# Kernel optimization log

Hardware: AMD Instinct MI355X
Metric: run time of the kernel (lower is better)

## Reference

```python
import jax, jax.numpy as jnp
import numpy as np
import math

E = 1024   # embedding_dim
H = 16     # num_attention_heads
DH = 64    # head_embedding_dim
THD = H * DH
EPS = 1e-5

def _layernorm(x, g, b):
    m = jnp.mean(x, axis=-1, keepdims=True)
    v = jnp.mean(jnp.square(x - m), axis=-1, keepdims=True)
    return (x - m) * jax.lax.rsqrt(v + EPS) * g + b

def setup_inputs() -> dict:
    key = jax.random.key(0)
    ks = jax.random.split(key, 16)
    s_in = 1.0 / math.sqrt(E)
    s_o = 1.0 / math.sqrt(THD)
    inp = {"tokens": jax.random.normal(ks[0], (2, 2048, E), dtype=jnp.float32)}
    # q_linear / k_linear / v_linear: LayerNorm(E) then Linear(E -> THD)
    for i, name in enumerate(["q", "k", "v"]):
        inp[f"ln_{name}_g"] = jnp.ones((E,), jnp.float32)
        inp[f"ln_{name}_b"] = jnp.zeros((E,), jnp.float32)
        inp[f"W{name}"] = jax.random.uniform(ks[1 + 2 * i], (E, THD), jnp.float32, -s_in, s_in)
        inp[f"b{name}"] = jax.random.uniform(ks[2 + 2 * i], (THD,), jnp.float32, -s_in, s_in)
    # attention_linear: LayerNorm(THD) then Linear(THD -> E)
    inp["ln_o_g"] = jnp.ones((THD,), jnp.float32)
    inp["ln_o_b"] = jnp.zeros((THD,), jnp.float32)
    inp["Wo"] = jax.random.uniform(ks[7], (THD, E), jnp.float32, -s_o, s_o)
    inp["bo"] = jax.random.uniform(ks[8], (E,), jnp.float32, -s_o, s_o)
    return inp

def reference(tokens, ln_q_g, ln_q_b, Wq, bq, ln_k_g, ln_k_b, Wk, bk,
              ln_v_g, ln_v_b, Wv, bv, ln_o_g, ln_o_b, Wo, bo):
    N, L, _ = tokens.shape
    # NOTE: faithful to source quirk -- k comes from v_linear, v comes from k_linear.
    q = (_layernorm(tokens, ln_q_g, ln_q_b) @ Wq + bq).reshape(N, L, H, DH).transpose(0, 2, 1, 3)  # (N,H,L,Dh)
    k = (_layernorm(tokens, ln_v_g, ln_v_b) @ Wv + bv).reshape(N, L, H, DH).transpose(0, 2, 3, 1)  # (N,H,Dh,L)
    v = (_layernorm(tokens, ln_k_g, ln_k_b) @ Wk + bk).reshape(N, L, H, DH).transpose(0, 2, 1, 3)  # (N,H,L,Dh)
    qkT = jnp.einsum('bhid,bhdj->bhij', q, k)  # (N,H,L,L)
    # mask added BEFORE dividing by sqrt(Dh), as in source
    mask = jnp.triu(jnp.full((L, L), -9999.0, dtype=qkT.dtype), k=1)
    attn = jax.nn.softmax((qkT + mask) / math.sqrt(DH), axis=-1)
    wv = jnp.einsum('bhij,bhjd->bhid', attn, v).transpose(0, 2, 1, 3).reshape(N, L, THD)
    out = _layernorm(wv, ln_o_g, ln_o_b) @ Wo + bo + tokens
    return (out, k, v)
```

## Files before the change

kernel.cpp:

```cpp
#include <hip/hip_runtime.h>

#define L_SEQ 2048
#define NH    16
#define E_DIM 1024
#define M_ROWS 4096

typedef unsigned short u16;
typedef unsigned int   u32;
typedef __attribute__((ext_vector_type(8))) __bf16 bf16x8;
typedef __attribute__((ext_vector_type(4))) float  f32x4;

__device__ __forceinline__ u16 f2bf(float f) {
  union { float f; u32 u; } x; x.f = f;
  u32 u = x.u;
  return (u16)((u + 0x7FFFu + ((u >> 16) & 1u)) >> 16);
}
__device__ __forceinline__ float bf2f(u16 v) {
  union { u32 u; float f; } x; x.u = ((u32)v) << 16;
  return x.f;
}
__device__ __forceinline__ void st_bf4(u16* p, float a, float b, float c, float d) {
  ushort4 u; u.x = f2bf(a); u.y = f2bf(b); u.z = f2bf(c); u.w = f2bf(d);
  *reinterpret_cast<ushort4*>(p) = u;
}
__device__ __forceinline__ u32 pktrunc(float a, float b) {
  union { float f; u32 u; } xa, xb; xa.f = a; xb.f = b;
  return (xa.u >> 16) | (xb.u & 0xFFFF0000u);
}
__device__ __forceinline__ void gload16(const u16* g, u16* l) {
  __builtin_amdgcn_global_load_lds(
      (const __attribute__((address_space(1))) void*)g,
      (__attribute__((address_space(3))) void*)l, 16, 0, 0);
}
#define SBAR() asm volatile("s_barrier" ::: "memory")

__global__ __launch_bounds__(256) void ln_hat_f32(const float* __restrict__ x, u16* __restrict__ o)
{
  __shared__ float red[8];
  const size_t row = blockIdx.x;
  const int t = threadIdx.x;
  float4 v = reinterpret_cast<const float4*>(x + row * E_DIM)[t];
  float s = v.x + v.y + v.z + v.w;
  float q = v.x*v.x + v.y*v.y + v.z*v.z + v.w*v.w;
  #pragma unroll
  for (int off = 32; off; off >>= 1) { s += __shfl_down(s, off); q += __shfl_down(q, off); }
  if ((t & 63) == 0) { red[t >> 6] = s; red[4 + (t >> 6)] = q; }
  __syncthreads();
  float S = red[0] + red[1] + red[2] + red[3];
  float Q = red[4] + red[5] + red[6] + red[7];
  float mean = S * (1.f / E_DIM);
  float rstd = rsqrtf(Q * (1.f / E_DIM) - mean * mean + 1e-5f);
  st_bf4(o + row * E_DIM + t * 4,
         (v.x - mean) * rstd, (v.y - mean) * rstd, (v.z - mean) * rstd, (v.w - mean) * rstd);
}

__global__ __launch_bounds__(256) void ln_hat_bf16(const u16* __restrict__ x, u16* __restrict__ o)
{
  __shared__ float red[8];
  const size_t row = blockIdx.x;
  const int t = threadIdx.x;
  ushort4 u = reinterpret_cast<const ushort4*>(x + row * E_DIM)[t];
  float v0 = bf2f(u.x), v1 = bf2f(u.y), v2 = bf2f(u.z), v3 = bf2f(u.w);
  float s = v0 + v1 + v2 + v3;
  float q = v0*v0 + v1*v1 + v2*v2 + v3*v3;
  #pragma unroll
  for (int off = 32; off; off >>= 1) { s += __shfl_down(s, off); q += __shfl_down(q, off); }
  if ((t & 63) == 0) { red[t >> 6] = s; red[4 + (t >> 6)] = q; }
  __syncthreads();
  float S = red[0] + red[1] + red[2] + red[3];
  float Q = red[4] + red[5] + red[6] + red[7];
  float mean = S * (1.f / E_DIM);
  float rstd = rsqrtf(Q * (1.f / E_DIM) - mean * mean + 1e-5f);
  st_bf4(o + row * E_DIM + t * 4,
         (v0 - mean) * rstd, (v1 - mean) * rstd, (v2 - mean) * rstd, (v3 - mean) * rstd);
}

__global__ __launch_bounds__(256) void transpose_all(
    const float* __restrict__ W0, const float* __restrict__ W1,
    const float* __restrict__ W2, const float* __restrict__ W3,
    const float* __restrict__ g0, const float* __restrict__ g1,
    const float* __restrict__ g2, const float* __restrict__ g3,
    u16* __restrict__ T0, u16* __restrict__ T1, u16* __restrict__ T2, u16* __restrict__ T3)
{
  __shared__ float tile[32][33];
  const int z = blockIdx.z;
  const float* W = (z == 0) ? W0 : (z == 1) ? W1 : (z == 2) ? W2 : W3;
  const float* g = (z == 0) ? g0 : (z == 1) ? g1 : (z == 2) ? g2 : g3;
  u16* T = (z == 0) ? T0 : (z == 1) ? T1 : (z == 2) ? T2 : T3;
  const int tx = threadIdx.x & 31, ty = threadIdx.x >> 5;
  const int bx = blockIdx.x * 32, by = blockIdx.y * 32;
  #pragma unroll
  for (int r = 0; r < 4; ++r) {
    const int e = by + ty + r * 8;
    tile[ty + r * 8][tx] = W[(size_t)e * E_DIM + bx + tx] * g[e];
  }
  __syncthreads();
  #pragma unroll
  for (int r = 0; r < 4; ++r)
    T[(size_t)(bx + ty + r * 8) * E_DIM + by + tx] = f2bf(tile[tx][ty + r * 8]);
}

__global__ __launch_bounds__(256) void bias_fold(
    const float* __restrict__ W0, const float* __restrict__ W1,
    const float* __restrict__ W2, const float* __restrict__ W3,
    const float* __restrict__ l0, const float* __restrict__ l1,
    const float* __restrict__ l2, const float* __restrict__ l3,
    const float* __restrict__ b0, const float* __restrict__ b1,
    const float* __restrict__ b2, const float* __restrict__ b3,
    float* __restrict__ bfold)
{
  __shared__ float part[8][32];
  const int z = blockIdx.y;
  const float* W  = (z == 0) ? W0 : (z == 1) ? W1 : (z == 2) ? W2 : W3;
  const float* bl = (z == 0) ? l0 : (z == 1) ? l1 : (z == 2) ? l2 : l3;
  const float* bs = (z == 0) ? b0 : (z == 1) ? b1 : (z == 2) ? b2 : b3;
  const int tn = threadIdx.x & 31, te = threadIdx.x >> 5;
  const int n = blockIdx.x * 32 + tn;
  float acc = 0.f;
  const int e0 = te * 128;
  for (int e = e0; e < e0 + 128; ++e) acc += bl[e] * W[(size_t)e * E_DIM + n];
  part[te][tn] = acc;
  __syncthreads();
  if (te == 0) {
    float s = part[0][tn] + part[1][tn] + part[2][tn] + part[3][tn]
            + part[4][tn] + part[5][tn] + part[6][tn] + part[7][tn];
    bfold[z * E_DIM + n] = bs[n] + s;
  }
}

#define GBK 64
__device__ __forceinline__ void core128(
    const u16* __restrict__ A, const u16* __restrict__ BT,
    int m0, int n0, int t, u16* lds, f32x4 (&acc)[4][4])
{
  const int lane = t & 63, wave = t >> 6;
  const int wm = wave >> 1, wn = wave & 1;
  const int fr = lane & 15, hi = lane >> 4;
  const int sx = fr & 7;

  auto STAGE = [&](int buf, int kt) {
    u16* la = lds + (buf * 2 + 0) * (128 * GBK);
    u16* lb = lds + (buf * 2 + 1) * (128 * GBK);
    #pragma unroll
    for (int s = 0; s < 4; ++s) {
      const int seg = t + s * 256;
      const int r = seg >> 3;
      const int gc = (seg & 7) ^ (r & 7);
      gload16(A + (size_t)(m0 + r) * E_DIM + kt * GBK + gc * 8, la + seg * 8);
    }
    #pragma unroll
    for (int s = 0; s < 4; ++s) {
      const int seg = t + s * 256;
      const int r = seg >> 3;
      const int gc = (seg & 7) ^ (r & 7);
      gload16(BT + (size_t)(n0 + r) * E_DIM + kt * GBK + gc * 8, lb + seg * 8);
    }
  };
  auto AF = [&](int buf, int i, int ks) -> bf16x8 {
    return *reinterpret_cast<const bf16x8*>(
        lds + (buf * 2 + 0) * (128 * GBK) + (wm * 64 + i * 16 + fr) * GBK + (((ks * 4 + hi) ^ sx) * 8));
  };
  auto BF = [&](int buf, int j, int ks) -> bf16x8 {
    return *reinterpret_cast<const bf16x8*>(
        lds + (buf * 2 + 1) * (128 * GBK) + (wn * 64 + j * 16 + fr) * GBK + (((ks * 4 + hi) ^ sx) * 8));
  };
  auto PHASES = [&](int buf) {
    bf16x8 a[4][2], b[4][2];
    #pragma unroll
    for (int i = 0; i < 4; ++i) { a[i][0] = AF(buf, i, 0); a[i][1] = AF(buf, i, 1); }
    #pragma unroll
    for (int j = 0; j < 4; ++j) { b[j][0] = BF(buf, j, 0); b[j][1] = BF(buf, j, 1); }
    __builtin_amdgcn_s_setprio(1);
    #pragma unroll
    for (int i = 0; i < 4; ++i)
      #pragma unroll
      for (int j = 0; j < 4; ++j) {
        acc[i][j] = __builtin_amdgcn_mfma_f32_16x16x32_bf16(a[i][0], b[j][0], acc[i][j], 0, 0, 0);
        acc[i][j] = __builtin_amdgcn_mfma_f32_16x16x32_bf16(a[i][1], b[j][1], acc[i][j], 0, 0, 0);
      }
    __builtin_amdgcn_s_setprio(0);
  };

  STAGE(0, 0);
  #pragma unroll 1
  for (int kt = 0; kt < 15; ++kt) {
    const int buf = kt & 1;
    SBAR();
    STAGE(buf ^ 1, kt + 1);
    asm volatile("s_waitcnt vmcnt(8)" ::: "memory");
    SBAR();
    PHASES(buf);
  }
  asm volatile("s_waitcnt vmcnt(0)" ::: "memory");
  SBAR();
  PHASES(1);
}

__global__ __launch_bounds__(256, 2) void gemm_qkv128(
    const u16* __restrict__ xhat, const u16* __restrict__ WTcat,
    const float* __restrict__ bfold,
    float* __restrict__ kout, float* __restrict__ vout,
    u16* __restrict__ qbf, u16* __restrict__ kbf, u16* __restrict__ vTb)
{
  __shared__ u16 lds[4 * 128 * GBK];
  const int t = threadIdx.x;
  const int xcd = blockIdx.x & 7, l = blockIdx.x >> 3;
  const int by = 8 * (xcd >> 1) + l / 12;
  const int bx = 12 * (xcd & 1) + l % 12;
  const int m0 = by * 128, n0 = bx * 128;

  f32x4 acc[4][4] = {};
  core128(xhat, WTcat, m0, n0, t, lds, acc);

  const int lane = t & 63, wave = t >> 6;
  const int wm = wave >> 1, wn = wave & 1;
  const int fr = lane & 15, hi = lane >> 4;
  const int z = n0 >> 10;
  const float* bias = bfold + z * E_DIM;
  const int rowb = hi * 4;
  #pragma unroll
  for (int i = 0; i < 4; ++i) {
    const int mbase = m0 + wm * 64 + i * 16 + rowb;
    #pragma unroll
    for (int j = 0; j < 4; ++j) {
      const int ng = n0 + wn * 64 + j * 16 + fr;
      const int ncol = ng & 1023;
      const float bval = bias[ncol];
      #pragma unroll
      for (int r = 0; r < 4; ++r) {
        const int m = mbase + r;
        const float val = acc[i][j][r] + bval;
        const int b = m >> 11, ltok = m & 2047, h = ncol >> 6, d = ncol & 63;
        const size_t bh = (size_t)(b * NH + h);
        if (z == 0) {
          qbf[((bh * L_SEQ + ltok) << 6) + d] = f2bf(val);
        } else if (z == 1) {
          kout[(bh * 64 + d) * L_SEQ + ltok] = val;
          kbf[((bh * L_SEQ + ltok) << 6) + d] = f2bf(val);
        } else {
          vout[(bh * L_SEQ + ltok) * 64 + d] = val;
          vTb[(bh * 64 + d) * L_SEQ + ltok] = f2bf(val);
        }
      }
    }
  }
}

__global__ __launch_bounds__(256, 2) void gemm_o128(
    const u16* __restrict__ A, const u16* __restrict__ BT, const float* __restrict__ bias,
    const float* __restrict__ tokens, float* __restrict__ out)
{
  __shared__ u16 lds[4 * 128 * GBK];
  const int t = threadIdx.x;
  const int xcd = blockIdx.x & 7, l = blockIdx.x >> 3;
  const int by = 8 * (xcd >> 1) + (l >> 2);
  const int bx = 4 * (xcd & 1) + (l & 3);
  const int m0 = by * 128, n0 = bx * 128;

  f32x4 acc[4][4] = {};
  core128(A, BT, m0, n0, t, lds, acc);

  const int lane = t & 63, wave = t >> 6;
  const int wm = wave >> 1, wn = wave & 1;
  const int fr = lane & 15, hi = lane >> 4;
  const int rowb = hi * 4;
  #pragma unroll
  for (int i = 0; i < 4; ++i) {
    const int mbase = m0 + wm * 64 + i * 16 + rowb;
    #pragma unroll
    for (int j = 0; j < 4; ++j) {
      const int ncol = n0 + wn * 64 + j * 16 + fr;
      const float bval = bias[ncol];
      #pragma unroll
      for (int r = 0; r < 4; ++r) {
        const int m = mbase + r;
        out[(size_t)m * E_DIM + ncol] = acc[i][j][r] + bval + tokens[(size_t)m * E_DIM + ncol];
      }
    }
  }
}

__global__ __launch_bounds__(256) void attn_mfma(
    const u16* __restrict__ qbf, const u16* __restrict__ kbf,
    const u16* __restrict__ vTb, u16* __restrict__ wv)
{
  __shared__ u16 Klds[64][72];
  __shared__ u16 Vlds[64][72];
  __shared__ u16 Plds[4][16][72];
  const int t = threadIdx.x, lane = t & 63, wave = t >> 6;
  const int bi = blockIdx.x;
  const int bh = (bi & 7) + 8 * ((bi >> 3) & 3);
  const int pr = bi >> 5;
  const int fr = lane & 15, hi = lane >> 4;
  const u16* kbase = kbf + (size_t)bh * L_SEQ * 64;
  const u16* vbase = vTb + (size_t)bh * 64 * L_SEQ;
  const int b = bh >> 4, h = bh & 15;
  const float kSC2  = 0.125f * 1.44269504089f;
  const float kMSK2 = -1803.2f;

  #pragma unroll 1
  for (int half = 0; half < 2; ++half) {
    const int qt = half ? (31 - pr) : pr;
    const int q0w = qt * 64 + wave * 16;
    const int qg = q0w + fr;

    const u16* qrow = qbf + ((size_t)bh * L_SEQ + q0w + fr) * 64 + hi * 8;
    const bf16x8 qf0 = *reinterpret_cast<const bf16x8*>(qrow);
    const bf16x8 qf1 = *reinterpret_cast<const bf16x8*>(qrow + 32);

    f32x4 o[4] = {};
    float mrun = -3.0e38f, lrun = 0.f;

    for (int tkv = 0; tkv <= qt; ++tkv) {
      const int j0 = tkv * 64;
      const bool diag = (tkv == qt);
      #pragma unroll
      for (int s = 0; s < 2; ++s) {
        const int seg = t + s * 256;
        const int r = seg >> 3, c8 = (seg & 7) * 8;
        *reinterpret_cast<uint4*>(&Klds[r][c8]) =
            *reinterpret_cast<const uint4*>(kbase + (size_t)(j0 + r) * 64 + c8);
        *reinterpret_cast<uint4*>(&Vlds[r][c8]) =
            *reinterpret_cast<const uint4*>(vbase + (size_t)r * L_SEQ + j0 + c8);
      }
      __syncthreads();

      f32x4 st[4] = {};
      __builtin_amdgcn_s_setprio(1);
      #pragma unroll
      for (int kt = 0; kt < 4; ++kt) {
        bf16x8 ka0 = *reinterpret_cast<const bf16x8*>(&Klds[kt*16 + fr][hi*8]);
        bf16x8 ka1 = *reinterpret_cast<const bf16x8*>(&Klds[kt*16 + fr][32 + hi*8]);
        st[kt] = __builtin_amdgcn_mfma_f32_16x16x32_bf16(ka0, qf0, st[kt], 0, 0, 0);
        st[kt] = __builtin_amdgcn_mfma_f32_16x16x32_bf16(ka1, qf1, st[kt], 0, 0, 0);
      }
      __builtin_amdgcn_s_setprio(0);

      float p[16];
      float pmax = -3.0e38f;
      #pragma unroll
      for (int kt = 0; kt < 4; ++kt)
        #pragma unroll
        for (int r = 0; r < 4; ++r) {
          const int key = j0 + kt*16 + hi*4 + r;
          const float v = st[kt][r] * kSC2 + ((diag && key > qg) ? kMSK2 : 0.f);
          p[kt*4 + r] = v;
          pmax = fmaxf(pmax, v);
        }
      pmax = fmaxf(pmax, __shfl_xor(pmax, 16));
      pmax = fmaxf(pmax, __shfl_xor(pmax, 32));
      if (!__all(pmax - mrun <= 8.f)) {
        const float mnew = fmaxf(mrun, pmax);
        const float alpha = exp2f(mrun - mnew);
        #pragma unroll
        for (int r = 0; r < 4; ++r) {
          const float ar = __shfl(alpha, hi*4 + r);
          o[0][r] *= ar; o[1][r] *= ar; o[2][r] *= ar; o[3][r] *= ar;
        }
        lrun *= alpha;
        mrun = mnew;
      }
      float lsum = 0.f;
      #pragma unroll
      for (int i = 0; i < 16; ++i) { p[i] = exp2f(p[i] - mrun); lsum += p[i]; }
      lsum += __shfl_xor(lsum, 16);
      lsum += __shfl_xor(lsum, 32);
      lrun += lsum;

      #pragma unroll
      for (int kt = 0; kt < 4; ++kt) {
        uint2 w2;
        w2.x = pktrunc(p[kt*4+0], p[kt*4+1]);
        w2.y = pktrunc(p[kt*4+2], p[kt*4+3]);
        *reinterpret_cast<uint2*>(&Plds[wave][fr][kt*16 + hi*4]) = w2;
      }

      const bf16x8 pf0 = *reinterpret_cast<const bf16x8*>(&Plds[wave][fr][hi*8]);
      const bf16x8 pf1 = *reinterpret_cast<const bf16x8*>(&Plds[wave][fr][32 + hi*8]);
      __builtin_amdgcn_s_setprio(1);
      #pragma unroll
      for (int dt = 0; dt < 4; ++dt) {
        bf16x8 vf0 = *reinterpret_cast<const bf16x8*>(&Vlds[dt*16 + fr][hi*8]);
        bf16x8 vf1 = *reinterpret_cast<const bf16x8*>(&Vlds[dt*16 + fr][32 + hi*8]);
        o[dt] = __builtin_amdgcn_mfma_f32_16x16x32_bf16(pf0, vf0, o[dt], 0, 0, 0);
        o[dt] = __builtin_amdgcn_mfma_f32_16x16x32_bf16(pf1, vf1, o[dt], 0, 0, 0);
      }
      __builtin_amdgcn_s_setprio(0);
      __syncthreads();
    }

    const float inv = 1.f / lrun;
    #pragma unroll
    for (int r = 0; r < 4; ++r) {
      const float ir = __shfl(inv, hi*4 + r);
      const int q = q0w + hi*4 + r;
      u16* dst = wv + (size_t)(b * L_SEQ + q) * E_DIM + h * 64 + fr;
      #pragma unroll
      for (int dt = 0; dt < 4; ++dt)
        dst[dt * 16] = f2bf(o[dt][r] * ir);
    }
  }
}

extern "C" void kernel_launch(void* const* d_in, const int* in_sizes, int n_in,
                              void* d_out, int out_size, void* d_ws, size_t ws_size,
                              hipStream_t stream) {
  (void)in_sizes; (void)n_in; (void)out_size; (void)ws_size;
  const float* tokens = (const float*)d_in[0];
  const float* ln_q_g = (const float*)d_in[1];
  const float* ln_q_b = (const float*)d_in[2];
  const float* Wq     = (const float*)d_in[3];
  const float* bq     = (const float*)d_in[4];
  const float* ln_k_g = (const float*)d_in[5];
  const float* ln_k_b = (const float*)d_in[6];
  const float* Wk     = (const float*)d_in[7];
  const float* bk     = (const float*)d_in[8];
  const float* ln_v_g = (const float*)d_in[9];
  const float* ln_v_b = (const float*)d_in[10];
  const float* Wv     = (const float*)d_in[11];
  const float* bv     = (const float*)d_in[12];
  const float* ln_o_g = (const float*)d_in[13];
  const float* ln_o_b = (const float*)d_in[14];
  const float* Wo     = (const float*)d_in[15];
  const float* bo     = (const float*)d_in[16];

  float* out  = (float*)d_out;
  float* kout = out + 4194304;
  float* vout = kout + 4194304;

  char* w = (char*)d_ws;
  const size_t MB = (size_t)1 << 20;
  u16*   WTq   = (u16*)(w + 0 * MB);
  u16*   WTv   = (u16*)(w + 2 * MB);
  u16*   WTk   = (u16*)(w + 4 * MB);
  u16*   WTo   = (u16*)(w + 6 * MB);
  u16*   xhat  = (u16*)(w + 8 * MB);
  u16*   qbf   = (u16*)(w + 16 * MB);
  u16*   kbf   = (u16*)(w + 24 * MB);
  u16*   vTb   = (u16*)(w + 32 * MB);
  u16*   what  = (u16*)(w + 40 * MB);
  float* bfold = (float*)(w + 48 * MB);
  u16*   wvb   = xhat;

  transpose_all<<<dim3(32, 32, 4), 256, 0, stream>>>(
      Wq, Wv, Wk, Wo, ln_q_g, ln_v_g, ln_k_g, ln_o_g, WTq, WTv, WTk, WTo);
  bias_fold<<<dim3(32, 4), 256, 0, stream>>>(
      Wq, Wv, Wk, Wo, ln_q_b, ln_v_b, ln_k_b, ln_o_b, bq, bv, bk, bo, bfold);
  ln_hat_f32<<<M_ROWS, 256, 0, stream>>>(tokens, xhat);
  gemm_qkv128<<<768, 256, 0, stream>>>(xhat, WTq, bfold, kout, vout, qbf, kbf, vTb);
  attn_mfma<<<512, 256, 0, stream>>>(qbf, kbf, vTb, wvb);
  ln_hat_bf16<<<M_ROWS, 256, 0, stream>>>(wvb, what);
  gemm_o128<<<256, 256, 0, stream>>>(what, WTo, bfold + 3 * E_DIM, tokens, out);
}
```

Before: 139.6 us.

## Share K/V tile loads between paired causal query tiles in attention kernel

The attention kernel used to process its two paired query tiles (pr and 31-pr) one after the other, reloading K/V tiles for each. Now it walks the KV sequence once for the longer tile and, while tkv <= pr, also updates the second tile's accumulators from the same LDS-resident K/V tile. This roughly halves global K/V loads and barriers per block. In exchange it doubles the per-thread accumulator and softmax state, which raises register pressure and may reduce occupancy.

Result: slower. 145.5 us (+4.2%).

```diff
diff --git a/kernel.cpp b/kernel.cpp
--- a/kernel.cpp
+++ b/kernel.cpp
@@ -298,41 +298,48 @@
   const float kSC2  = 0.125f * 1.44269504089f;
   const float kMSK2 = -1803.2f;
 
+  const int qtA = 31 - pr;
+  const int qtB = pr;
+  const int q0wA = qtA * 64 + wave * 16;
+  const int q0wB = qtB * 64 + wave * 16;
+  const int qgA = q0wA + fr;
+  const int qgB = q0wB + fr;
+
+  const u16* qrowA = qbf + ((size_t)bh * L_SEQ + q0wA + fr) * 64 + hi * 8;
+  const bf16x8 qfA0 = *reinterpret_cast<const bf16x8*>(qrowA);
+  const bf16x8 qfA1 = *reinterpret_cast<const bf16x8*>(qrowA + 32);
+  const u16* qrowB = qbf + ((size_t)bh * L_SEQ + q0wB + fr) * 64 + hi * 8;
+  const bf16x8 qfB0 = *reinterpret_cast<const bf16x8*>(qrowB);
+  const bf16x8 qfB1 = *reinterpret_cast<const bf16x8*>(qrowB + 32);
+
+  f32x4 oA[4] = {}, oB[4] = {};
+  float mA = -3.0e38f, lA = 0.f;
+  float mB = -3.0e38f, lB = 0.f;
+
   #pragma unroll 1
-  for (int half = 0; half < 2; ++half) {
-    const int qt = half ? (31 - pr) : pr;
-    const int q0w = qt * 64 + wave * 16;
-    const int qg = q0w + fr;
-
-    const u16* qrow = qbf + ((size_t)bh * L_SEQ + q0w + fr) * 64 + hi * 8;
-    const bf16x8 qf0 = *reinterpret_cast<const bf16x8*>(qrow);
-    const bf16x8 qf1 = *reinterpret_cast<const bf16x8*>(qrow + 32);
-
-    f32x4 o[4] = {};
-    float mrun = -3.0e38f, lrun = 0.f;
-
-    for (int tkv = 0; tkv <= qt; ++tkv) {
-      const int j0 = tkv * 64;
-      const bool diag = (tkv == qt);
-      #pragma unroll
-      for (int s = 0; s < 2; ++s) {
-        const int seg = t + s * 256;
-        const int r = seg >> 3, c8 = (seg & 7) * 8;
-        *reinterpret_cast<uint4*>(&Klds[r][c8]) =
-            *reinterpret_cast<const uint4*>(kbase + (size_t)(j0 + r) * 64 + c8);
-        *reinterpret_cast<uint4*>(&Vlds[r][c8]) =
-            *reinterpret_cast<const uint4*>(vbase + (size_t)r * L_SEQ + j0 + c8);
-      }
-      __syncthreads();
-
+  for (int tkv = 0; tkv <= qtA; ++tkv) {
+    const int j0 = tkv * 64;
+    #pragma unroll
+    for (int s = 0; s < 2; ++s) {
+      const int seg = t + s * 256;
+      const int r = seg >> 3, c8 = (seg & 7) * 8;
+      *reinterpret_cast<uint4*>(&Klds[r][c8]) =
+          *reinterpret_cast<const uint4*>(kbase + (size_t)(j0 + r) * 64 + c8);
+      *reinterpret_cast<uint4*>(&Vlds[r][c8]) =
+          *reinterpret_cast<const uint4*>(vbase + (size_t)r * L_SEQ + j0 + c8);
+    }
+    __syncthreads();
+
+    {
+      const bool diag = (tkv == qtA);
       f32x4 st[4] = {};
       __builtin_amdgcn_s_setprio(1);
       #pragma unroll
       for (int kt = 0; kt < 4; ++kt) {
         bf16x8 ka0 = *reinterpret_cast<const bf16x8*>(&Klds[kt*16 + fr][hi*8]);
         bf16x8 ka1 = *reinterpret_cast<const bf16x8*>(&Klds[kt*16 + fr][32 + hi*8]);
-        st[kt] = __builtin_amdgcn_mfma_f32_16x16x32_bf16(ka0, qf0, st[kt], 0, 0, 0);
-        st[kt] = __builtin_amdgcn_mfma_f32_16x16x32_bf16(ka1, qf1, st[kt], 0, 0, 0);
+        st[kt] = __builtin_amdgcn_mfma_f32_16x16x32_bf16(ka0, qfA0, st[kt], 0, 0, 0);
+        st[kt] = __builtin_amdgcn_mfma_f32_16x16x32_bf16(ka1, qfA1, st[kt], 0, 0, 0);
       }
       __builtin_amdgcn_s_setprio(0);
 
@@ -343,29 +350,29 @@
         #pragma unroll
         for (int r = 0; r < 4; ++r) {
           const int key = j0 + kt*16 + hi*4 + r;
-          const float v = st[kt][r] * kSC2 + ((diag && key > qg) ? kMSK2 : 0.f);
+          const float v = st[kt][r] * kSC2 + ((diag && key > qgA) ? kMSK2 : 0.f);
           p[kt*4 + r] = v;
           pmax = fmaxf(pmax, v);
         }
       pmax = fmaxf(pmax, __shfl_xor(pmax, 16));
       pmax = fmaxf(pmax, __shfl_xor(pmax, 32));
-      if (!__all(pmax - mrun <= 8.f)) {
-        const float mnew = fmaxf(mrun, pmax);
-        const float alpha = exp2f(mrun - mnew);
+      if (!__all(pmax - mA <= 8.f)) {
+        const float mnew = fmaxf(mA, pmax);
+        const float alpha = exp2f(mA - mnew);
         #pragma unroll
         for (int r = 0; r < 4; ++r) {
           const float ar = __shfl(alpha, hi*4 + r);
-          o[0][r] *= ar; o[1][r] *= ar; o[2][r] *= ar; o[3][r] *= ar;
+          oA[0][r] *= ar; oA[1][r] *= ar; oA[2][r] *= ar; oA[3][r] *= ar;
         }
-        lrun *= alpha;
-        mrun = mnew;
+        lA *= alpha;
+        mA = mnew;
       }
       float lsum = 0.f;
       #pragma unroll
-      for (int i = 0; i < 16; ++i) { p[i] = exp2f(p[i] - mrun); lsum += p[i]; }
+      for (int i = 0; i < 16; ++i) { p[i] = exp2f(p[i] - mA); lsum += p[i]; }
       lsum += __shfl_xor(lsum, 16);
       lsum += __shfl_xor(lsum, 32);
-      lrun += lsum;
+      lA += lsum;
 
       #pragma unroll
       for (int kt = 0; kt < 4; ++kt) {
@@ -374,7 +381,6 @@
         w2.y = pktrunc(p[kt*4+2], p[kt*4+3]);
         *reinterpret_cast<uint2*>(&Plds[wave][fr][kt*16 + hi*4]) = w2;
       }
-
       const bf16x8 pf0 = *reinterpret_cast<const bf16x8*>(&Plds[wave][fr][hi*8]);
       const bf16x8 pf1 = *reinterpret_cast<const bf16x8*>(&Plds[wave][fr][32 + hi*8]);
       __builtin_amdgcn_s_setprio(1);
@@ -382,22 +388,100 @@
       for (int dt = 0; dt < 4; ++dt) {
         bf16x8 vf0 = *reinterpret_cast<const bf16x8*>(&Vlds[dt*16 + fr][hi*8]);
         bf16x8 vf1 = *reinterpret_cast<const bf16x8*>(&Vlds[dt*16 + fr][32 + hi*8]);
-        o[dt] = __builtin_amdgcn_mfma_f32_16x16x32_bf16(pf0, vf0, o[dt], 0, 0, 0);
-        o[dt] = __builtin_amdgcn_mfma_f32_16x16x32_bf16(pf1, vf1, o[dt], 0, 0, 0);
+        oA[dt] = __builtin_amdgcn_mfma_f32_16x16x32_bf16(pf0, vf0, oA[dt], 0, 0, 0);
+        oA[dt] = __builtin_amdgcn_mfma_f32_16x16x32_bf16(pf1, vf1, oA[dt], 0, 0, 0);
       }
       __builtin_amdgcn_s_setprio(0);
-      __syncthreads();
-    }
-
-    const float inv = 1.f / lrun;
+    }
+
+    if (tkv <= qtB) {
+      const bool diag = (tkv == qtB);
+      f32x4 st[4] = {};
+      __builtin_amdgcn_s_setprio(1);
+      #pragma unroll
+      for (int kt = 0; kt < 4; ++kt) {
+        bf16x8 ka0 = *reinterpret_cast<const bf16x8*>(&Klds[kt*16 + fr][hi*8]);
+        bf16x8 ka1 = *reinterpret_cast<const bf16x8*>(&Klds[kt*16 + fr][32 + hi*8]);
+        st[kt] = __builtin_amdgcn_mfma_f32_16x16x32_bf16(ka0, qfB0, st[kt], 0, 0, 0);
+        st[kt] = __builtin_amdgcn_mfma_f32_16x16x32_bf16(ka1, qfB1, st[kt], 0, 0, 0);
+      }
+      __builtin_amdgcn_s_setprio(0);
+
+      float p[16];
+      float pmax = -3.0e38f;
+      #pragma unroll
+      for (int kt = 0; kt < 4; ++kt)
+        #pragma unroll
+        for (int r = 0; r < 4; ++r) {
+          const int key = j0 + kt*16 + hi*4 + r;
+          const float v = st[kt][r] * kSC2 + ((diag && key > qgB) ? kMSK2 : 0.f);
+          p[kt*4 + r] = v;
+          pmax = fmaxf(pmax, v);
+        }
+      pmax = fmaxf(pmax, __shfl_xor(pmax, 16));
+      pmax = fmaxf(pmax, __shfl_xor(pmax, 32));
+      if (!__all(pmax - mB <= 8.f)) {
+        const float mnew = fmaxf(mB, pmax);
+        const float alpha = exp2f(mB - mnew);
+        #pragma unroll
+        for (int r = 0; r < 4; ++r) {
+          const float ar = __shfl(alpha, hi*4 + r);
+          oB[0][r] *= ar; oB[1][r] *= ar; oB[2][r] *= ar; oB[3][r] *= ar;
+        }
+        lB *= alpha;
+        mB = mnew;
+      }
+      float lsum = 0.f;
+      #pragma unroll
+      for (int i = 0; i < 16; ++i) { p[i] = exp2f(p[i] - mB); lsum += p[i]; }
+      lsum += __shfl_xor(lsum, 16);
+      lsum += __shfl_xor(lsum, 32);
+      lB += lsum;
+
+      #pragma unroll
+      for (int kt = 0; kt < 4; ++kt) {
+        uint2 w2;
+        w2.x = pktrunc(p[kt*4+0], p[kt*4+1]);
+        w2.y = pktrunc(p[kt*4+2], p[kt*4+3]);
+        *reinterpret_cast<uint2*>(&Plds[wave][fr][kt*16 + hi*4]) = w2;
+      }
+      const bf16x8 pf0 = *reinterpret_cast<const bf16x8*>(&Plds[wave][fr][hi*8]);
+      const bf16x8 pf1 = *reinterpret_cast<const bf16x8*>(&Plds[wave][fr][32 + hi*8]);
+      __builtin_amdgcn_s_setprio(1);
+      #pragma unroll
+      for (int dt = 0; dt < 4; ++dt) {
+        bf16x8 vf0 = *reinterpret_cast<const bf16x8*>(&Vlds[dt*16 + fr][hi*8]);
+        bf16x8 vf1 = *reinterpret_cast<const bf16x8*>(&Vlds[dt*16 + fr][32 + hi*8]);
+        oB[dt] = __builtin_amdgcn_mfma_f32_16x16x32_bf16(pf0, vf0, oB[dt], 0, 0, 0);
+        oB[dt] = __builtin_amdgcn_mfma_f32_16x16x32_bf16(pf1, vf1, oB[dt], 0, 0, 0);
+      }
+      __builtin_amdgcn_s_setprio(0);
+    }
+    __syncthreads();
+  }
+
+  {
+    const float inv = 1.f / lA;
     #pragma unroll
     for (int r = 0; r < 4; ++r) {
       const float ir = __shfl(inv, hi*4 + r);
-      const int q = q0w + hi*4 + r;
+      const int q = q0wA + hi*4 + r;
       u16* dst = wv + (size_t)(b * L_SEQ + q) * E_DIM + h * 64 + fr;
       #pragma unroll
       for (int dt = 0; dt < 4; ++dt)
-        dst[dt * 16] = f2bf(o[dt][r] * ir);
+        dst[dt * 16] = f2bf(oA[dt][r] * ir);
+    }
+  }
+  {
+    const float inv = 1.f / lB;
+    #pragma unroll
+    for (int r = 0; r < 4; ++r) {
+      const float ir = __shfl(inv, hi*4 + r);
+      const int q = q0wB + hi*4 + r;
+      u16* dst = wv + (size_t)(b * L_SEQ + q) * E_DIM + h * 64 + fr;
+      #pragma unroll
+      for (int dt = 0; dt < 4; ++dt)
+        dst[dt * 16] = f2bf(oB[dt][r] * ir);
     }
   }
 }
```
